# Performance work log

Measured on AMD Instinct MI355X. Metric: run time of the kernel, lower is better.

The kernel has to match this reference:

```python
import jax, jax.numpy as jnp
import numpy as np

D_MODEL = 256
D_FFN = 1024
N_LEVELS = 4
N_HEADS = 8
N_POINTS = 4
HEAD_DIM = D_MODEL // N_HEADS
SPATIAL = [(128, 128), (64, 64), (32, 32), (16, 16)]
LQ = sum(h * w for h, w in SPATIAL)  # 21760
B = 2


def setup_inputs() -> dict:
    key = jax.random.key(0)
    ks = jax.random.split(key, 24)

    def w(k, shape, s=0.02):
        return (jax.random.normal(k, shape) * s).astype(jnp.float32)

    HLP = N_HEADS * N_LEVELS * N_POINTS
    starts = np.cumsum([0] + [h * w_ for h, w_ in SPATIAL[:-1]])
    return {
        "src": jax.random.normal(ks[0], (B, LQ, D_MODEL), jnp.float32),
        "pos": 0.1 * jax.random.normal(ks[1], (B, LQ, D_MODEL), jnp.float32),
        "reference_points": jax.random.uniform(ks[2], (B, LQ, N_LEVELS, 2), jnp.float32),
        "W_off": w(ks[3], (D_MODEL, HLP * 2)),
        "b_off": w(ks[4], (HLP * 2,), 0.5),
        "W_attn": w(ks[5], (D_MODEL, HLP)),
        "b_attn": jnp.zeros((HLP,), jnp.float32),
        "W_val": w(ks[6], (D_MODEL, D_MODEL)),
        "b_val": jnp.zeros((D_MODEL,), jnp.float32),
        "W_out": w(ks[7], (D_MODEL, D_MODEL)),
        "b_out": jnp.zeros((D_MODEL,), jnp.float32),
        "ln1_g": jnp.ones((D_MODEL,), jnp.float32),
        "ln1_b": jnp.zeros((D_MODEL,), jnp.float32),
        "W1": w(ks[8], (D_MODEL, D_FFN)),
        "b1": jnp.zeros((D_FFN,), jnp.float32),
        "W2": w(ks[9], (D_FFN, D_MODEL)),
        "b2": jnp.zeros((D_MODEL,), jnp.float32),
        "ln2_g": jnp.ones((D_MODEL,), jnp.float32),
        "ln2_b": jnp.zeros((D_MODEL,), jnp.float32),
        "spatial_shapes": np.array(SPATIAL, np.int32),
        "level_start_index": np.array(starts, np.int32),
    }


def _layernorm(x, g, b):
    mu = x.mean(-1, keepdims=True)
    var = ((x - mu) ** 2).mean(-1, keepdims=True)
    return (x - mu) * jax.lax.rsqrt(var + 1e-5) * g + b


def _bilinear_sample(v, x, y, H, W):
    # v: [N, H, W, D]; x, y: [N, Lq, P] pixel coords (align_corners=False, zero pad)
    x0f = jnp.floor(x)
    y0f = jnp.floor(y)
    x0 = x0f.astype(jnp.int32)
    y0 = y0f.astype(jnp.int32)
    wx1 = x - x0f
    wy1 = y - y0f
    wx0 = 1.0 - wx1
    wy0 = 1.0 - wy1
    vf = v.reshape(v.shape[0], H * W, v.shape[-1])

    def gather(xi, yi, wt):
        valid = (xi >= 0) & (xi < W) & (yi >= 0) & (yi < H)
        idx = jnp.clip(yi, 0, H - 1) * W + jnp.clip(xi, 0, W - 1)
        g = jnp.take_along_axis(vf, idx.reshape(idx.shape[0], -1)[..., None], axis=1)
        g = g.reshape(*xi.shape, vf.shape[-1])
        return g * (wt * valid.astype(wt.dtype))[..., None]

    return (gather(x0, y0, wx0 * wy0) + gather(x0 + 1, y0, wx1 * wy0)
            + gather(x0, y0 + 1, wx0 * wy1) + gather(x0 + 1, y0 + 1, wx1 * wy1))


def _ms_deform_attn(query, src, reference_points, W_off, b_off, W_attn, b_attn,
                    W_val, b_val, W_out, b_out, spatial_shapes):
    Bq, Lq, _ = query.shape
    ss = np.asarray(spatial_shapes)
    value = (src @ W_val + b_val).reshape(Bq, Lq, N_HEADS, HEAD_DIM)
    off = (query @ W_off + b_off).reshape(Bq, Lq, N_HEADS, N_LEVELS, N_POINTS, 2)
    attn = (query @ W_attn + b_attn).reshape(Bq, Lq, N_HEADS, N_LEVELS * N_POINTS)
    attn = jax.nn.softmax(attn, axis=-1).reshape(Bq, Lq, N_HEADS, N_LEVELS, N_POINTS)
    # offset normalizer = (W, H) per level
    normalizer = jnp.asarray(ss[:, ::-1].astype(np.float32))  # [L, 2]
    loc = reference_points[:, :, None, :, None, :] + off / normalizer[None, None, None, :, None, :]
    # loc: [B, Lq, M, L, P, 2] normalized in [0,1]
    out = jnp.zeros((Bq, N_HEADS, Lq, HEAD_DIM), query.dtype)
    start = 0
    for lvl in range(N_LEVELS):
        H, W = int(ss[lvl, 0]), int(ss[lvl, 1])
        v = value[:, start:start + H * W]                                 # [B, HW, M, D]
        v = v.transpose(0, 2, 1, 3).reshape(Bq * N_HEADS, H, W, HEAD_DIM)
        l = loc[:, :, :, lvl]                                             # [B, Lq, M, P, 2]
        x = (l[..., 0] * W - 0.5).transpose(0, 2, 1, 3).reshape(Bq * N_HEADS, Lq, N_POINTS)
        y = (l[..., 1] * H - 0.5).transpose(0, 2, 1, 3).reshape(Bq * N_HEADS, Lq, N_POINTS)
        sampled = _bilinear_sample(v, x, y, H, W)                         # [BM, Lq, P, D]
        wgt = attn[:, :, :, lvl].transpose(0, 2, 1, 3).reshape(Bq * N_HEADS, Lq, N_POINTS)
        out = out + (sampled * wgt[..., None]).sum(2).reshape(Bq, N_HEADS, Lq, HEAD_DIM)
        start += H * W
    out = out.transpose(0, 2, 1, 3).reshape(Bq, Lq, D_MODEL)
    return out @ W_out + b_out


def reference(src, pos, reference_points, W_off, b_off, W_attn, b_attn, W_val, b_val,
              W_out, b_out, ln1_g, ln1_b, W1, b1, W2, b2, ln2_g, ln2_b,
              spatial_shapes, level_start_index):
    query = src + pos
    src2 = _ms_deform_attn(query, src, reference_points, W_off, b_off, W_attn, b_attn,
                           W_val, b_val, W_out, b_out, spatial_shapes)
    h = _layernorm(src + src2, ln1_g, ln1_b)
    ffn = jax.nn.relu(h @ W1 + b1) @ W2 + b2
    return _layernorm(h + ffn, ln2_g, ln2_b)
```

## Files before the change

### kernel.cpp

```cpp
#include <hip/hip_runtime.h>

typedef __bf16 bf16x8 __attribute__((ext_vector_type(8)));
typedef float f32x4 __attribute__((ext_vector_type(4)));
typedef float f32x2 __attribute__((ext_vector_type(2)));

static constexpr int TOKS = 43520;
static constexpr int LQN  = 21760;

__device__ __forceinline__ unsigned short f2bf(float f) {
  union { float f; unsigned u; } v; v.f = f;
  return (unsigned short)((v.u + 0x7fffu + ((v.u >> 16) & 1u)) >> 16);
}
__device__ __forceinline__ float bf2f(unsigned short b) {
  union { unsigned u; float f; } v; v.u = ((unsigned)b) << 16; return v.f;
}

__global__ __launch_bounds__(256) void prewt_kernel(
    const float* __restrict__ src, const float* __restrict__ pos,
    unsigned short* __restrict__ srcb, unsigned short* __restrict__ qb,
    const float* __restrict__ W_val, const float* __restrict__ W_off,
    const float* __restrict__ W_attn, const float* __restrict__ W_out,
    const float* __restrict__ W1, const float* __restrict__ W2,
    const float* __restrict__ b_off, const float* __restrict__ b_attn,
    unsigned short* __restrict__ Wt_val, unsigned short* __restrict__ Wt_oa,
    unsigned short* __restrict__ Wt_out,
    unsigned short* __restrict__ Wt_1, unsigned short* __restrict__ Wt_2,
    float* __restrict__ b_oa) {
  const int bid = blockIdx.x;
  const int t = threadIdx.x;
  if (bid < 10880) {
    int i = bid * 256 + t;
    float4 s = ((const float4*)src)[i], p = ((const float4*)pos)[i];
    ((ushort4*)srcb)[i] = make_ushort4(f2bf(s.x), f2bf(s.y), f2bf(s.z), f2bf(s.w));
    ((ushort4*)qb)[i]   = make_ushort4(f2bf(s.x + p.x), f2bf(s.y + p.y),
                                       f2bf(s.z + p.z), f2bf(s.w + p.w));
    return;
  }
  if (bid == 11616) {
    b_oa[t] = (t < 256) ? b_off[t] : 0.f;
    if (t >= 256) return;
    if (t < 128) b_oa[256 + t] = b_attn[t];
    return;
  }
  int tid = bid - 10880;
  const float* W; unsigned short* Wt; int Kd, Nd, nshn;
  if (tid < 64)        {            W = W_val;  Wt = Wt_val;         Kd = 256;  Nd = 256;  nshn = 3; }
  else if (tid < 128)  { tid -= 64; W = W_off;  Wt = Wt_oa;          Kd = 256;  Nd = 256;  nshn = 3; }
  else if (tid < 160)  { tid -= 128;W = W_attn; Wt = Wt_oa + 65536;  Kd = 256;  Nd = 128;  nshn = 2; }
  else if (tid < 224)  { tid -= 160;W = W_out;  Wt = Wt_out;         Kd = 256;  Nd = 256;  nshn = 3; }
  else if (tid < 480)  { tid -= 224;W = W1;     Wt = Wt_1;           Kd = 256;  Nd = 1024; nshn = 5; }
  else                 { tid -= 480;W = W2;     Wt = Wt_2;           Kd = 1024; Nd = 256;  nshn = 3; }
  const int k0 = (tid >> nshn) * 32;
  const int n0 = (tid & ((1 << nshn) - 1)) * 32;
  __shared__ float tileT[32][33];
  {
    const int kl = t >> 3, nc = (t & 7) * 4;
    float4 v = *(const float4*)&W[(size_t)(k0 + kl) * Nd + n0 + nc];
    tileT[nc + 0][kl] = v.x; tileT[nc + 1][kl] = v.y;
    tileT[nc + 2][kl] = v.z; tileT[nc + 3][kl] = v.w;
  }
  __syncthreads();
  {
    const int nl = t >> 3, kc = (t & 7) * 4;
    ushort4 o = make_ushort4(f2bf(tileT[nl][kc + 0]), f2bf(tileT[nl][kc + 1]),
                             f2bf(tileT[nl][kc + 2]), f2bf(tileT[nl][kc + 3]));
    *(ushort4*)&Wt[(size_t)(n0 + nl) * Kd + k0 + kc] = o;
  }
}

template <int K, int OUTOP>
__device__ __forceinline__ void gemm_body(unsigned short* __restrict__ As,
                                          unsigned short* __restrict__ Bs,
                                          const unsigned short* __restrict__ A,
                                          const unsigned short* __restrict__ Bt,
                                          const float* __restrict__ bias,
                                          const unsigned short* __restrict__ res,
                                          unsigned short* __restrict__ Cp,
                                          int N, int bm, int bn) {
  const int t = threadIdx.x;
  const int wave = t >> 6, lane = t & 63;
  const int wm = (wave & 1) << 6, wn = (wave >> 1) << 6;
  const int lr = lane & 15, lq = lane >> 4;
  const int row0 = t >> 2, cb0 = (t & 3) << 3;
  f32x4 acc[4][4] = {};
  const unsigned short* ga = A  + (size_t)(bm * 128 + row0) * K + cb0;
  const unsigned short* gb = Bt + (size_t)(bn * 128 + row0) * K + cb0;
  const size_t gs = (size_t)64 * K;
  uint4 pa0 = *(const uint4*)ga;
  uint4 pa1 = *(const uint4*)(ga + gs);
  uint4 pb0 = *(const uint4*)gb;
  uint4 pb1 = *(const uint4*)(gb + gs);
  int p = 0;
#pragma unroll 1
  for (int k0 = 0; k0 < K; k0 += 32) {
    unsigned short* Ab = As + p * 5120;
    unsigned short* Bb = Bs + p * 5120;
    *(uint4*)&Ab[row0 * 40 + cb0] = pa0;
    *(uint4*)&Ab[(row0 + 64) * 40 + cb0] = pa1;
    *(uint4*)&Bb[row0 * 40 + cb0] = pb0;
    *(uint4*)&Bb[(row0 + 64) * 40 + cb0] = pb1;
    __syncthreads();
    if (k0 + 32 < K) {
      pa0 = *(const uint4*)(ga + k0 + 32);
      pa1 = *(const uint4*)(ga + gs + k0 + 32);
      pb0 = *(const uint4*)(gb + k0 + 32);
      pb1 = *(const uint4*)(gb + gs + k0 + 32);
    }
    bf16x8 af[4], bfr[4];
#pragma unroll
    for (int i = 0; i < 4; i++) af[i] = *(const bf16x8*)&Ab[(wm + i * 16 + lr) * 40 + lq * 8];
#pragma unroll
    for (int j = 0; j < 4; j++) bfr[j] = *(const bf16x8*)&Bb[(wn + j * 16 + lr) * 40 + lq * 8];
#pragma unroll
    for (int i = 0; i < 4; i++)
#pragma unroll
      for (int j = 0; j < 4; j++)
        acc[i][j] = __builtin_amdgcn_mfma_f32_16x16x32_bf16(af[i], bfr[j], acc[i][j], 0, 0, 0);
    p ^= 1;
  }
  const int rb = bm * 128 + wm + lq * 4;
  const int cbase = bn * 128 + wn + lr;
#pragma unroll
  for (int j = 0; j < 4; j++) {
    const int col = cbase + j * 16;
    const float bv = bias[col];
#pragma unroll
    for (int i = 0; i < 4; i++) {
#pragma unroll
      for (int r = 0; r < 4; r++) {
        float v = acc[i][j][r] + bv;
        size_t o = (size_t)(rb + i * 16 + r) * N + col;
        if (OUTOP == 1) Cp[o] = f2bf(v);
        else if (OUTOP == 2) Cp[o] = f2bf(fmaxf(v, 0.f));
        else Cp[o] = f2bf(v + bf2f(res[o]));
      }
    }
  }
}

__global__ __launch_bounds__(256) void proj_kernel(
    const unsigned short* __restrict__ srcb, const unsigned short* __restrict__ qb,
    const unsigned short* __restrict__ Wt_val, const unsigned short* __restrict__ Wt_oa,
    const float* __restrict__ b_val, const float* __restrict__ b_oa,
    unsigned short* __restrict__ valb, unsigned short* __restrict__ oab) {
  __shared__ unsigned short As[2 * 5120];
  __shared__ unsigned short Bs[2 * 5120];
  const int bn = blockIdx.y;
  if (bn < 2)
    gemm_body<256, 1>(As, Bs, srcb, Wt_val, b_val, nullptr, valb, 256, blockIdx.x, bn);
  else
    gemm_body<256, 1>(As, Bs, qb, Wt_oa, b_oa, nullptr, oab, 384, blockIdx.x, bn - 2);
}

__global__ __launch_bounds__(256, 3) void fused_tail_kernel(
    const unsigned short* __restrict__ attn,
    const unsigned short* __restrict__ Wot,
    const float* __restrict__ b_out,
    const unsigned short* __restrict__ srcres,
    const float* __restrict__ g1, const float* __restrict__ be1,
    const unsigned short* __restrict__ W1t,
    const unsigned short* __restrict__ W2t,
    const float* __restrict__ b1, const float* __restrict__ b2,
    const float* __restrict__ g2, const float* __restrict__ be2,
    float* __restrict__ out) {
  __shared__ unsigned short Ah[64 * 264];
  __shared__ unsigned short Hc[64 * 136];
  __shared__ float red[2][4][64];
  const int t = threadIdx.x;
  const int w = t >> 6, lane = t & 63;
  const int lr = lane & 15, lq = lane >> 4;
  const size_t rowbase = (size_t)blockIdx.x * 64;

  {
    const uint4* gsrc = (const uint4*)(attn + rowbase * 256);
#pragma unroll
    for (int u = 0; u < 8; u++) {
      const int idx = u * 256 + t;
      const int row = idx >> 5, c8 = idx & 31;
      *(uint4*)&Ah[row * 264 + c8 * 8] = gsrc[idx];
    }
  }
  __syncthreads();

  f32x4 acc0[4][4] = {};
  {
    const size_t wb = (size_t)(w * 64 + lr) * 256 + lq * 8;
    bf16x8 wf0[2][4];
#pragma unroll
    for (int d = 0; d < 2; d++)
#pragma unroll
      for (int j = 0; j < 4; j++)
        wf0[d][j] = *(const bf16x8*)&Wot[wb + (size_t)j * 4096 + d * 32];
#pragma unroll
    for (int ks = 0; ks < 8; ks++) {
      bf16x8 c0 = wf0[ks & 1][0], c1 = wf0[ks & 1][1];
      bf16x8 c2 = wf0[ks & 1][2], c3 = wf0[ks & 1][3];
      if (ks + 2 < 8) {
#pragma unroll
        for (int j = 0; j < 4; j++)
          wf0[ks & 1][j] = *(const bf16x8*)&Wot[wb + (size_t)j * 4096 + (ks + 2) * 32];
      }
      bf16x8 af[4];
#pragma unroll
      for (int i = 0; i < 4; i++)
        af[i] = *(const bf16x8*)&Ah[(i * 16 + lr) * 264 + ks * 32 + lq * 8];
#pragma unroll
      for (int i = 0; i < 4; i++) {
        acc0[i][0] = __builtin_amdgcn_mfma_f32_16x16x32_bf16(af[i], c0, acc0[i][0], 0, 0, 0);
        acc0[i][1] = __builtin_amdgcn_mfma_f32_16x16x32_bf16(af[i], c1, acc0[i][1], 0, 0, 0);
        acc0[i][2] = __builtin_amdgcn_mfma_f32_16x16x32_bf16(af[i], c2, acc0[i][2], 0, 0, 0);
        acc0[i][3] = __builtin_amdgcn_mfma_f32_16x16x32_bf16(af[i], c3, acc0[i][3], 0, 0, 0);
      }
    }
  }
  {
    float vsum[4][4], vsq[4][4];
#pragma unroll
    for (int i = 0; i < 4; i++)
#pragma unroll
      for (int r = 0; r < 4; r++) { vsum[i][r] = 0.f; vsq[i][r] = 0.f; }
#pragma unroll
    for (int j = 0; j < 4; j++) {
      const int col = w * 64 + j * 16 + lr;
      const float bv = b_out[col];
#pragma unroll
      for (int i = 0; i < 4; i++)
#pragma unroll
        for (int r = 0; r < 4; r++) {
          const int row = i * 16 + lq * 4 + r;
          float v = acc0[i][j][r] + bv + bf2f(srcres[(rowbase + row) * 256 + col]);
          acc0[i][j][r] = v;
          vsum[i][r] += v;
          vsq[i][r]  += v * v;
        }
    }
#pragma unroll
    for (int m = 1; m <= 8; m <<= 1)
#pragma unroll
      for (int i = 0; i < 4; i++)
#pragma unroll
        for (int r = 0; r < 4; r++) {
          vsum[i][r] += __shfl_xor(vsum[i][r], m, 64);
          vsq[i][r]  += __shfl_xor(vsq[i][r],  m, 64);
        }
    if (lr == 0) {
#pragma unroll
      for (int i = 0; i < 4; i++)
#pragma unroll
        for (int r = 0; r < 4; r++) {
          const int row = i * 16 + lq * 4 + r;
          red[0][w][row] = vsum[i][r];
          red[1][w][row] = vsq[i][r];
        }
    }
    __syncthreads();
    float mu[4][4], rstd[4][4];
#pragma unroll
    for (int i = 0; i < 4; i++)
#pragma unroll
      for (int r = 0; r < 4; r++) {
        const int row = i * 16 + lq * 4 + r;
        const float ts = red[0][0][row] + red[0][1][row] + red[0][2][row] + red[0][3][row];
        const float tq = red[1][0][row] + red[1][1][row] + red[1][2][row] + red[1][3][row];
        const float m_ = ts * (1.f / 256.f);
        mu[i][r] = m_;
        rstd[i][r] = rsqrtf(tq * (1.f / 256.f) - m_ * m_ + 1e-5f);
      }
#pragma unroll
    for (int j = 0; j < 4; j++) {
      const int col = w * 64 + j * 16 + lr;
      const float gg = g1[col], bb = be1[col];
#pragma unroll
      for (int i = 0; i < 4; i++)
#pragma unroll
        for (int r = 0; r < 4; r++) {
          const int row = i * 16 + lq * 4 + r;
          const float y = (acc0[i][j][r] - mu[i][r]) * rstd[i][r] * gg + bb;
          Ah[row * 264 + col] = f2bf(y);
        }
    }
  }
  __syncthreads();

  f32x4 acc2[4][4] = {};
  const int c1base = w * 32;
#pragma unroll 1
  for (int c2 = 0; c2 < 8; c2++) {
    f32x4 acc1[4][2] = {};
    const size_t w1r0 = (size_t)(c2 * 128 + c1base + lr) * 256 + lq * 8;
    const size_t w1r1 = w1r0 + (size_t)16 * 256;
    bf16x8 wf[4][2];
#pragma unroll
    for (int d = 0; d < 4; d++) {
      wf[d][0] = *(const bf16x8*)&W1t[w1r0 + d * 32];
      wf[d][1] = *(const bf16x8*)&W1t[w1r1 + d * 32];
    }
#pragma unroll
    for (int ks = 0; ks < 8; ks++) {
      bf16x8 b0 = wf[ks & 3][0], b1v = wf[ks & 3][1];
      if (ks + 4 < 8) {
        wf[ks & 3][0] = *(const bf16x8*)&W1t[w1r0 + (ks + 4) * 32];
        wf[ks & 3][1] = *(const bf16x8*)&W1t[w1r1 + (ks + 4) * 32];
      }
      bf16x8 af[4];
#pragma unroll
      for (int i = 0; i < 4; i++)
        af[i] = *(const bf16x8*)&Ah[(i * 16 + lr) * 264 + ks * 32 + lq * 8];
#pragma unroll
      for (int i = 0; i < 4; i++) {
        acc1[i][0] = __builtin_amdgcn_mfma_f32_16x16x32_bf16(af[i], b0,  acc1[i][0], 0, 0, 0);
        acc1[i][1] = __builtin_amdgcn_mfma_f32_16x16x32_bf16(af[i], b1v, acc1[i][1], 0, 0, 0);
      }
    }
    __syncthreads();
#pragma unroll
    for (int j = 0; j < 2; j++) {
      const int colc = c1base + j * 16 + lr;
      const float bv = b1[c2 * 128 + colc];
#pragma unroll
      for (int i = 0; i < 4; i++)
#pragma unroll
        for (int r = 0; r < 4; r++)
          Hc[(i * 16 + lq * 4 + r) * 136 + colc] = f2bf(fmaxf(acc1[i][j][r] + bv, 0.f));
    }
    __syncthreads();
    const size_t w2b = (size_t)(w * 64 + lr) * 1024 + c2 * 128 + lq * 8;
    bf16x8 wg[2][4];
#pragma unroll
    for (int d = 0; d < 2; d++)
#pragma unroll
      for (int j = 0; j < 4; j++)
        wg[d][j] = *(const bf16x8*)&W2t[w2b + (size_t)j * 16384 + d * 32];
#pragma unroll
    for (int ks = 0; ks < 4; ks++) {
      bf16x8 c0 = wg[ks & 1][0], c1 = wg[ks & 1][1];
      bf16x8 cc2 = wg[ks & 1][2], c3 = wg[ks & 1][3];
      if (ks + 2 < 4) {
#pragma unroll
        for (int j = 0; j < 4; j++)
          wg[ks & 1][j] = *(const bf16x8*)&W2t[w2b + (size_t)j * 16384 + (ks + 2) * 32];
      }
      bf16x8 af2[4];
#pragma unroll
      for (int i = 0; i < 4; i++)
        af2[i] = *(const bf16x8*)&Hc[(i * 16 + lr) * 136 + ks * 32 + lq * 8];
#pragma unroll
      for (int i = 0; i < 4; i++) {
        acc2[i][0] = __builtin_amdgcn_mfma_f32_16x16x32_bf16(af2[i], c0,  acc2[i][0], 0, 0, 0);
        acc2[i][1] = __builtin_amdgcn_mfma_f32_16x16x32_bf16(af2[i], c1,  acc2[i][1], 0, 0, 0);
        acc2[i][2] = __builtin_amdgcn_mfma_f32_16x16x32_bf16(af2[i], cc2, acc2[i][2], 0, 0, 0);
        acc2[i][3] = __builtin_amdgcn_mfma_f32_16x16x32_bf16(af2[i], c3,  acc2[i][3], 0, 0, 0);
      }
    }
  }
  float vsum[4][4], vsq[4][4];
#pragma unroll
  for (int i = 0; i < 4; i++)
#pragma unroll
    for (int r = 0; r < 4; r++) { vsum[i][r] = 0.f; vsq[i][r] = 0.f; }
#pragma unroll
  for (int j = 0; j < 4; j++) {
    const int col = w * 64 + j * 16 + lr;
    const float bv = b2[col];
#pragma unroll
    for (int i = 0; i < 4; i++)
#pragma unroll
      for (int r = 0; r < 4; r++) {
        const int row = i * 16 + lq * 4 + r;
        float v = acc2[i][j][r] + bv + bf2f(Ah[row * 264 + col]);
        acc2[i][j][r] = v;
        vsum[i][r] += v;
        vsq[i][r]  += v * v;
      }
  }
#pragma unroll
  for (int m = 1; m <= 8; m <<= 1)
#pragma unroll
    for (int i = 0; i < 4; i++)
#pragma unroll
      for (int r = 0; r < 4; r++) {
        vsum[i][r] += __shfl_xor(vsum[i][r], m, 64);
        vsq[i][r]  += __shfl_xor(vsq[i][r],  m, 64);
      }
  __syncthreads();
  if (lr == 0) {
#pragma unroll
    for (int i = 0; i < 4; i++)
#pragma unroll
      for (int r = 0; r < 4; r++) {
        const int row = i * 16 + lq * 4 + r;
        red[0][w][row] = vsum[i][r];
        red[1][w][row] = vsq[i][r];
      }
  }
  __syncthreads();
  float mu[4][4], rstd[4][4];
#pragma unroll
  for (int i = 0; i < 4; i++)
#pragma unroll
    for (int r = 0; r < 4; r++) {
      const int row = i * 16 + lq * 4 + r;
      const float ts = red[0][0][row] + red[0][1][row] + red[0][2][row] + red[0][3][row];
      const float tq = red[1][0][row] + red[1][1][row] + red[1][2][row] + red[1][3][row];
      const float m_ = ts * (1.f / 256.f);
      mu[i][r] = m_;
      rstd[i][r] = rsqrtf(tq * (1.f / 256.f) - m_ * m_ + 1e-5f);
    }
#pragma unroll
  for (int j = 0; j < 4; j++) {
    const int col = w * 64 + j * 16 + lr;
    const float gg = g2[col], bb = be2[col];
#pragma unroll
    for (int i = 0; i < 4; i++)
#pragma unroll
      for (int r = 0; r < 4; r++) {
        const int row = i * 16 + lq * 4 + r;
        out[(rowbase + row) * 256 + col] = (acc2[i][j][r] - mu[i][r]) * rstd[i][r] * gg + bb;
      }
  }
}

__device__ __forceinline__ void fma8(uint4 v, float w, f32x2* a) {
  const unsigned uu[4] = {v.x, v.y, v.z, v.w};
  const f32x2 w2 = {w, w};
#pragma unroll
  for (int i = 0; i < 4; i++) {
    union { unsigned u; float f; } lo, hi;
    lo.u = uu[i] << 16;
    hi.u = uu[i] & 0xffff0000u;
    f32x2 val = {lo.f, hi.f};
    a[i] += w2 * val;
  }
}

__global__ __launch_bounds__(256) void deform_kernel(const unsigned short* __restrict__ valb,
                                                     const unsigned short* __restrict__ oab,
                                                     const float* __restrict__ refp,
                                                     unsigned short* __restrict__ outb) {
  __shared__ float4 sW[8][8][17];
  __shared__ int4   sI[8][8][17];
  const int t = threadIdx.x;
  const int bid = blockIdx.x;
  const int nb = (bid & 7) * 680 + (bid >> 3);
  const int tok0 = nb * 8;

  {
    const int g = t >> 5, h = (t >> 2) & 7, l = t & 3;
    const int tok = tok0 + g;
    const unsigned short* lg = oab + (size_t)tok * 384 + 256 + h * 16;
    uint4 lv0 = ((const uint4*)lg)[0];
    uint4 lv1 = ((const uint4*)lg)[1];
    const unsigned lw[8] = {lv0.x, lv0.y, lv0.z, lv0.w, lv1.x, lv1.y, lv1.z, lv1.w};
    float w[16];
#pragma unroll
    for (int i = 0; i < 8; i++) {
      union { unsigned u; float f; } lo, hi;
      lo.u = lw[i] << 16; hi.u = lw[i] & 0xffff0000u;
      w[2 * i] = lo.f; w[2 * i + 1] = hi.f;
    }
    float mx = -1e30f;
#pragma unroll
    for (int i = 0; i < 16; i++) mx = fmaxf(mx, w[i]);
    float s = 0.f;
#pragma unroll
    for (int i = 0; i < 16; i++) { w[i] = __expf(w[i] - mx); s += w[i]; }
    const float inv = 1.f / s;
    uint4 ov = *(const uint4*)(oab + (size_t)tok * 384 + h * 32 + l * 8);
    const unsigned owv[4] = {ov.x, ov.y, ov.z, ov.w};
    float off[8];
#pragma unroll
    for (int i = 0; i < 4; i++) {
      union { unsigned u; float f; } lo, hi;
      lo.u = owv[i] << 16; hi.u = owv[i] & 0xffff0000u;
      off[2 * i] = lo.f; off[2 * i + 1] = hi.f;
    }
    const float* rp = refp + (size_t)tok * 8 + l * 2;
    const int S = 128 >> l;
    const float Sf = (float)S;
    const float rx = rp[0] * Sf - 0.5f;
    const float ry = rp[1] * Sf - 0.5f;
#pragma unroll
    for (int p = 0; p < 4; p++) {
      const int idx = l * 4 + p;
      const float x = rx + off[p * 2 + 0];
      const float y = ry + off[p * 2 + 1];
      const float aw = w[idx] * inv;
      const float x0f = floorf(x), y0f = floorf(y);
      const int x0 = (int)x0f, y0 = (int)y0f;
      const float fx = x - x0f, fy = y - y0f;
      const bool xin0 = (x0 >= 0) & (x0 < S), xin1 = (x0 + 1 >= 0) & (x0 + 1 < S);
      const bool yin0 = (y0 >= 0) & (y0 < S), yin1 = (y0 + 1 >= 0) & (y0 + 1 < S);
      const int xc0 = min(max(x0, 0), S - 1), xc1 = min(max(x0 + 1, 0), S - 1);
      const int yc0 = min(max(y0, 0), S - 1), yc1 = min(max(y0 + 1, 0), S - 1);
      sW[g][h][idx] = make_float4(aw * (1.f - fx) * (1.f - fy) * (float)(xin0 & yin0),
                                  aw * fx * (1.f - fy)         * (float)(xin1 & yin0),
                                  aw * (1.f - fx) * fy         * (float)(xin0 & yin1),
                                  aw * fx * fy                 * (float)(xin1 & yin1));
      sI[g][h][idx] = make_int4((yc0 * S + xc0) << 9, (yc0 * S + xc1) << 9,
                                (yc1 * S + xc0) << 9, (yc1 * S + xc1) << 9);
    }
  }
  __syncthreads();

  const int g = t >> 5, h = (t >> 2) & 7, dc = t & 3;
  const int tok = tok0 + g;
  const int b = tok / LQN;
  f32x2 acc[4] = {};
  const int ST[4] = {0, 16384, 20480, 21504};
#pragma unroll
  for (int l = 0; l < 4; l++) {
    const char* vbc = (const char*)(valb + ((size_t)(b * LQN + ST[l])) * 256 + h * 32 + dc * 8);
#pragma unroll
    for (int p = 0; p < 4; p++) {
      float4 W4 = sW[g][h][l * 4 + p];
      int4   I4 = sI[g][h][l * 4 + p];
      uint4 v00 = *(const uint4*)(vbc + I4.x);
      uint4 v10 = *(const uint4*)(vbc + I4.y);
      uint4 v01 = *(const uint4*)(vbc + I4.z);
      uint4 v11 = *(const uint4*)(vbc + I4.w);
      fma8(v00, W4.x, acc);
      fma8(v10, W4.y, acc);
      fma8(v01, W4.z, acc);
      fma8(v11, W4.w, acc);
    }
  }
  unsigned o[4];
#pragma unroll
  for (int i = 0; i < 4; i++)
    o[i] = (unsigned)f2bf(acc[i].x) | ((unsigned)f2bf(acc[i].y) << 16);
  *(uint4*)(outb + (size_t)tok * 256 + h * 32 + dc * 8) = make_uint4(o[0], o[1], o[2], o[3]);
}

extern "C" void kernel_launch(void* const* d_in, const int* in_sizes, int n_in,
                              void* d_out, int out_size, void* d_ws, size_t ws_size,
                              hipStream_t stream) {
  (void)in_sizes; (void)n_in; (void)out_size; (void)ws_size;
  const float* src    = (const float*)d_in[0];
  const float* pos    = (const float*)d_in[1];
  const float* refp   = (const float*)d_in[2];
  const float* W_off  = (const float*)d_in[3];
  const float* b_off  = (const float*)d_in[4];
  const float* W_attn = (const float*)d_in[5];
  const float* b_attn = (const float*)d_in[6];
  const float* W_val  = (const float*)d_in[7];
  const float* b_val  = (const float*)d_in[8];
  const float* W_out  = (const float*)d_in[9];
  const float* b_out  = (const float*)d_in[10];
  const float* ln1_g  = (const float*)d_in[11];
  const float* ln1_b  = (const float*)d_in[12];
  const float* W1     = (const float*)d_in[13];
  const float* b1     = (const float*)d_in[14];
  const float* W2     = (const float*)d_in[15];
  const float* b2     = (const float*)d_in[16];
  const float* ln2_g  = (const float*)d_in[17];
  const float* ln2_b  = (const float*)d_in[18];

  char* ws = (char*)d_ws;
  unsigned short* Wt_val = (unsigned short*)ws;
  unsigned short* Wt_oa  = Wt_val + 65536;
  unsigned short* Wt_out = Wt_oa + 98304;
  unsigned short* Wt_1   = Wt_out + 65536;
  unsigned short* Wt_2   = Wt_1 + 262144;
  float*          b_oa   = (float*)(Wt_2 + 262144);
  const size_t WPOOL = 2u * 1024 * 1024;

  const size_t SZ_bf = (size_t)TOKS * 256 * 2;
  const size_t SZ_oa = (size_t)TOKS * 384 * 2;

  unsigned short* srcb = (unsigned short*)(ws + WPOOL);
  unsigned short* qb   = (unsigned short*)(ws + WPOOL + SZ_bf);
  unsigned short* valb = (unsigned short*)(ws + WPOOL + 2 * SZ_bf);
  unsigned short* oab  = (unsigned short*)(ws + WPOOL + 3 * SZ_bf);
  unsigned short* attnoutb = qb;

  prewt_kernel<<<11617, 256, 0, stream>>>(src, pos, srcb, qb,
                                          W_val, W_off, W_attn, W_out, W1, W2, b_off, b_attn,
                                          Wt_val, Wt_oa, Wt_out, Wt_1, Wt_2, b_oa);

  proj_kernel<<<dim3(340, 5), 256, 0, stream>>>(srcb, qb, Wt_val, Wt_oa, b_val, b_oa,
                                                valb, oab);

  deform_kernel<<<TOKS / 8, 256, 0, stream>>>(valb, oab, refp, attnoutb);

  fused_tail_kernel<<<680, 256, 0, stream>>>(attnoutb, Wt_out, b_out, srcb, ln1_g, ln1_b,
                                             Wt_1, Wt_2, b1, b2, ln2_g, ln2_b,
                                             (float*)d_out);
}
```

Baseline: 429.7 us.

## Fuse fp32-to-bf16 conversion and pos add into projection GEMM loads

The separate pass that converted src and src+pos to bf16 is removed from the prep kernel. The projection GEMM now loads fp32 src/pos directly, adds pos and converts to bf16 on the fly while staging tiles into LDS. One column block also writes the bf16 src copy that the tail kernel needs for its residual. This avoids a full write and read of the bf16 query buffer, but the GEMM now reads twice as many bytes per A tile, and the src/pos rows are re-read for each column block (up to 3 for pos).

Measured after the change: 433.9 us. Within noise of the previous version (+1.0%).

```diff
diff --git a/kernel.cpp b/kernel.cpp
--- a/kernel.cpp
+++ b/kernel.cpp
@@ -14,10 +14,14 @@
 __device__ __forceinline__ float bf2f(unsigned short b) {
   union { unsigned u; float f; } v; v.u = ((unsigned)b) << 16; return v.f;
 }
+__device__ __forceinline__ ushort4 c4(float4 v) {
+  return make_ushort4(f2bf(v.x), f2bf(v.y), f2bf(v.z), f2bf(v.w));
+}
+__device__ __forceinline__ float4 add4(float4 a, float4 b) {
+  return make_float4(a.x + b.x, a.y + b.y, a.z + b.z, a.w + b.w);
+}
 
 __global__ __launch_bounds__(256) void prewt_kernel(
-    const float* __restrict__ src, const float* __restrict__ pos,
-    unsigned short* __restrict__ srcb, unsigned short* __restrict__ qb,
     const float* __restrict__ W_val, const float* __restrict__ W_off,
     const float* __restrict__ W_attn, const float* __restrict__ W_out,
     const float* __restrict__ W1, const float* __restrict__ W2,
@@ -28,21 +32,12 @@
     float* __restrict__ b_oa) {
   const int bid = blockIdx.x;
   const int t = threadIdx.x;
-  if (bid < 10880) {
-    int i = bid * 256 + t;
-    float4 s = ((const float4*)src)[i], p = ((const float4*)pos)[i];
-    ((ushort4*)srcb)[i] = make_ushort4(f2bf(s.x), f2bf(s.y), f2bf(s.z), f2bf(s.w));
-    ((ushort4*)qb)[i]   = make_ushort4(f2bf(s.x + p.x), f2bf(s.y + p.y),
-                                       f2bf(s.z + p.z), f2bf(s.w + p.w));
-    return;
-  }
-  if (bid == 11616) {
-    b_oa[t] = (t < 256) ? b_off[t] : 0.f;
-    if (t >= 256) return;
+  if (bid == 736) {
+    b_oa[t] = b_off[t];
     if (t < 128) b_oa[256 + t] = b_attn[t];
     return;
   }
-  int tid = bid - 10880;
+  int tid = bid;
   const float* W; unsigned short* Wt; int Kd, Nd, nshn;
   if (tid < 64)        {            W = W_val;  Wt = Wt_val;         Kd = 256;  Nd = 256;  nshn = 3; }
   else if (tid < 128)  { tid -= 64; W = W_off;  Wt = Wt_oa;          Kd = 256;  Nd = 256;  nshn = 3; }
@@ -68,41 +63,71 @@
   }
 }
 
-template <int K, int OUTOP>
-__device__ __forceinline__ void gemm_body(unsigned short* __restrict__ As,
+template <bool ADDPOS, bool WRITESRC>
+__device__ __forceinline__ void proj_body(unsigned short* __restrict__ As,
                                           unsigned short* __restrict__ Bs,
-                                          const unsigned short* __restrict__ A,
+                                          const float* __restrict__ A0,
+                                          const float* __restrict__ A1,
                                           const unsigned short* __restrict__ Bt,
                                           const float* __restrict__ bias,
-                                          const unsigned short* __restrict__ res,
                                           unsigned short* __restrict__ Cp,
-                                          int N, int bm, int bn) {
+                                          unsigned short* __restrict__ srcb_out,
+                                          int N, int bm, int bnw) {
   const int t = threadIdx.x;
   const int wave = t >> 6, lane = t & 63;
   const int wm = (wave & 1) << 6, wn = (wave >> 1) << 6;
   const int lr = lane & 15, lq = lane >> 4;
   const int row0 = t >> 2, cb0 = (t & 3) << 3;
   f32x4 acc[4][4] = {};
-  const unsigned short* ga = A  + (size_t)(bm * 128 + row0) * K + cb0;
-  const unsigned short* gb = Bt + (size_t)(bn * 128 + row0) * K + cb0;
-  const size_t gs = (size_t)64 * K;
-  uint4 pa0 = *(const uint4*)ga;
-  uint4 pa1 = *(const uint4*)(ga + gs);
+  const size_t arow = (size_t)(bm * 128 + row0) * 256 + cb0;
+  const float* ga0 = A0 + arow;
+  const float* ga1 = A0 + arow + (size_t)64 * 256;
+  const float* gp0 = A1 + arow;
+  const float* gp1 = A1 + arow + (size_t)64 * 256;
+  const unsigned short* gb = Bt + (size_t)(bnw * 128 + row0) * 256 + cb0;
+  const size_t gs = (size_t)64 * 256;
+
+  float4 fa0 = *(const float4*)ga0, fa1 = *(const float4*)(ga0 + 4);
+  float4 fa2 = *(const float4*)ga1, fa3 = *(const float4*)(ga1 + 4);
+  float4 fp0, fp1, fp2, fp3;
+  if (ADDPOS) {
+    fp0 = *(const float4*)gp0; fp1 = *(const float4*)(gp0 + 4);
+    fp2 = *(const float4*)gp1; fp3 = *(const float4*)(gp1 + 4);
+  }
   uint4 pb0 = *(const uint4*)gb;
   uint4 pb1 = *(const uint4*)(gb + gs);
   int p = 0;
 #pragma unroll 1
-  for (int k0 = 0; k0 < K; k0 += 32) {
+  for (int k0 = 0; k0 < 256; k0 += 32) {
+    float4 v0 = fa0, v1 = fa1, v2 = fa2, v3 = fa3;
+    if (ADDPOS) { v0 = add4(v0, fp0); v1 = add4(v1, fp1); v2 = add4(v2, fp2); v3 = add4(v3, fp3); }
+    ushort4 u0 = c4(v0), u1 = c4(v1), u2 = c4(v2), u3 = c4(v3);
     unsigned short* Ab = As + p * 5120;
     unsigned short* Bb = Bs + p * 5120;
-    *(uint4*)&Ab[row0 * 40 + cb0] = pa0;
-    *(uint4*)&Ab[(row0 + 64) * 40 + cb0] = pa1;
+    *(ushort4*)&Ab[row0 * 40 + cb0] = u0;
+    *(ushort4*)&Ab[row0 * 40 + cb0 + 4] = u1;
+    *(ushort4*)&Ab[(row0 + 64) * 40 + cb0] = u2;
+    *(ushort4*)&Ab[(row0 + 64) * 40 + cb0 + 4] = u3;
     *(uint4*)&Bb[row0 * 40 + cb0] = pb0;
     *(uint4*)&Bb[(row0 + 64) * 40 + cb0] = pb1;
+    if (WRITESRC) {
+      *(ushort4*)&srcb_out[arow + k0] = u0;
+      *(ushort4*)&srcb_out[arow + k0 + 4] = u1;
+      *(ushort4*)&srcb_out[arow + (size_t)64 * 256 + k0] = u2;
+      *(ushort4*)&srcb_out[arow + (size_t)64 * 256 + k0 + 4] = u3;
+    }
     __syncthreads();
-    if (k0 + 32 < K) {
-      pa0 = *(const uint4*)(ga + k0 + 32);
-      pa1 = *(const uint4*)(ga + gs + k0 + 32);
+    if (k0 + 32 < 256) {
+      fa0 = *(const float4*)(ga0 + k0 + 32);
+      fa1 = *(const float4*)(ga0 + k0 + 36);
+      fa2 = *(const float4*)(ga1 + k0 + 32);
+      fa3 = *(const float4*)(ga1 + k0 + 36);
+      if (ADDPOS) {
+        fp0 = *(const float4*)(gp0 + k0 + 32);
+        fp1 = *(const float4*)(gp0 + k0 + 36);
+        fp2 = *(const float4*)(gp1 + k0 + 32);
+        fp3 = *(const float4*)(gp1 + k0 + 36);
+      }
       pb0 = *(const uint4*)(gb + k0 + 32);
       pb1 = *(const uint4*)(gb + gs + k0 + 32);
     }
@@ -119,37 +144,34 @@
     p ^= 1;
   }
   const int rb = bm * 128 + wm + lq * 4;
-  const int cbase = bn * 128 + wn + lr;
+  const int cbase = bnw * 128 + wn + lr;
 #pragma unroll
   for (int j = 0; j < 4; j++) {
     const int col = cbase + j * 16;
     const float bv = bias[col];
 #pragma unroll
-    for (int i = 0; i < 4; i++) {
-#pragma unroll
-      for (int r = 0; r < 4; r++) {
-        float v = acc[i][j][r] + bv;
-        size_t o = (size_t)(rb + i * 16 + r) * N + col;
-        if (OUTOP == 1) Cp[o] = f2bf(v);
-        else if (OUTOP == 2) Cp[o] = f2bf(fmaxf(v, 0.f));
-        else Cp[o] = f2bf(v + bf2f(res[o]));
-      }
-    }
+    for (int i = 0; i < 4; i++)
+#pragma unroll
+      for (int r = 0; r < 4; r++)
+        Cp[(size_t)(rb + i * 16 + r) * N + col] = f2bf(acc[i][j][r] + bv);
   }
 }
 
 __global__ __launch_bounds__(256) void proj_kernel(
-    const unsigned short* __restrict__ srcb, const unsigned short* __restrict__ qb,
+    const float* __restrict__ src, const float* __restrict__ pos,
     const unsigned short* __restrict__ Wt_val, const unsigned short* __restrict__ Wt_oa,
     const float* __restrict__ b_val, const float* __restrict__ b_oa,
-    unsigned short* __restrict__ valb, unsigned short* __restrict__ oab) {
+    unsigned short* __restrict__ valb, unsigned short* __restrict__ oab,
+    unsigned short* __restrict__ srcb) {
   __shared__ unsigned short As[2 * 5120];
   __shared__ unsigned short Bs[2 * 5120];
   const int bn = blockIdx.y;
-  if (bn < 2)
-    gemm_body<256, 1>(As, Bs, srcb, Wt_val, b_val, nullptr, valb, 256, blockIdx.x, bn);
+  if (bn == 0)
+    proj_body<false, true>(As, Bs, src, src, Wt_val, b_val, valb, srcb, 256, blockIdx.x, 0);
+  else if (bn == 1)
+    proj_body<false, false>(As, Bs, src, src, Wt_val, b_val, valb, nullptr, 256, blockIdx.x, 1);
   else
-    gemm_body<256, 1>(As, Bs, qb, Wt_oa, b_oa, nullptr, oab, 384, blockIdx.x, bn - 2);
+    proj_body<true, false>(As, Bs, src, pos, Wt_oa, b_oa, oab, nullptr, 384, blockIdx.x, bn - 2);
 }
 
 __global__ __launch_bounds__(256, 3) void fused_tail_kernel(
@@ -565,20 +587,17 @@
   const size_t WPOOL = 2u * 1024 * 1024;
 
   const size_t SZ_bf = (size_t)TOKS * 256 * 2;
-  const size_t SZ_oa = (size_t)TOKS * 384 * 2;
-
-  unsigned short* srcb = (unsigned short*)(ws + WPOOL);
-  unsigned short* qb   = (unsigned short*)(ws + WPOOL + SZ_bf);
-  unsigned short* valb = (unsigned short*)(ws + WPOOL + 2 * SZ_bf);
-  unsigned short* oab  = (unsigned short*)(ws + WPOOL + 3 * SZ_bf);
-  unsigned short* attnoutb = qb;
-
-  prewt_kernel<<<11617, 256, 0, stream>>>(src, pos, srcb, qb,
-                                          W_val, W_off, W_attn, W_out, W1, W2, b_off, b_attn,
-                                          Wt_val, Wt_oa, Wt_out, Wt_1, Wt_2, b_oa);
-
-  proj_kernel<<<dim3(340, 5), 256, 0, stream>>>(srcb, qb, Wt_val, Wt_oa, b_val, b_oa,
-                                                valb, oab);
+
+  unsigned short* srcb     = (unsigned short*)(ws + WPOOL);
+  unsigned short* attnoutb = (unsigned short*)(ws + WPOOL + SZ_bf);
+  unsigned short* valb     = (unsigned short*)(ws + WPOOL + 2 * SZ_bf);
+  unsigned short* oab      = (unsigned short*)(ws + WPOOL + 3 * SZ_bf);
+
+  prewt_kernel<<<737, 256, 0, stream>>>(W_val, W_off, W_attn, W_out, W1, W2, b_off, b_attn,
+                                        Wt_val, Wt_oa, Wt_out, Wt_1, Wt_2, b_oa);
+
+  proj_kernel<<<dim3(340, 5), 256, 0, stream>>>(src, pos, Wt_val, Wt_oa, b_val, b_oa,
+                                                valb, oab, srcb);
 
   deform_kernel<<<TOKS / 8, 256, 0, stream>>>(valb, oab, refp, attnoutb);
 
```
